# Kernel optimization log

Hardware: AMD Instinct MI355X
Metric: run time of the kernel (lower is better)

The kernel has to match this reference:

```python
import jax, jax.numpy as jnp
import numpy as np
from functools import partial

SEQ, B, IN, H, L = 2048, 48, 128, 256, 2


def _lstm_layer(x_seq, Wih, Whh, bih, bhh):
    # x_seq: [S, B, in_dim]; PyTorch gate order i, f, g, o along 4H axis.
    Bsz = x_seq.shape[1]
    h0 = jnp.zeros((Bsz, Whh.shape[1]), x_seq.dtype)
    c0 = jnp.zeros_like(h0)
    bias = bih + bhh

    def step(carry, x_t):
        h, c = carry
        gates = x_t @ Wih.T + h @ Whh.T + bias  # [B, 4H]
        i, f, g, o = jnp.split(gates, 4, axis=-1)
        i = jax.nn.sigmoid(i)
        f = jax.nn.sigmoid(f)
        g = jnp.tanh(g)
        o = jax.nn.sigmoid(o)
        c = f * c + i * g
        h = o * jnp.tanh(c)
        return (h, c), h

    (h_n, c_n), ys = jax.lax.scan(step, (h0, c0), x_seq)
    return ys, h_n


def setup_inputs() -> dict:
    key = jax.random.key(0)
    ks = jax.random.split(key, 11)
    s_in = 1.0 / np.sqrt(H)

    def u(k, shape):
        return jax.random.uniform(k, shape, jnp.float32, -s_in, s_in)

    return {
        "x": jax.random.normal(ks[0], (SEQ, B, IN), jnp.float32),
        "W_ih0": u(ks[1], (4 * H, IN)),
        "W_hh0": u(ks[2], (4 * H, H)),
        "b_ih0": u(ks[3], (4 * H,)),
        "b_hh0": u(ks[4], (4 * H,)),
        "W_ih1": u(ks[5], (4 * H, H)),
        "W_hh1": u(ks[6], (4 * H, H)),
        "b_ih1": u(ks[7], (4 * H,)),
        "b_hh1": u(ks[8], (4 * H,)),
        "fc_w": u(ks[9], (1, H)),
        "fc_b": u(ks[10], (1,)),
    }


def reference(x, W_ih0, W_hh0, b_ih0, b_hh0, W_ih1, W_hh1, b_ih1, b_hh1, fc_w, fc_b):
    y0, h0n = _lstm_layer(x, W_ih0, W_hh0, b_ih0, b_hh0)   # [S,B,H]
    y1, h1n = _lstm_layer(y0, W_ih1, W_hh1, b_ih1, b_hh1)  # [S,B,H]
    hn = jnp.stack([h0n, h1n], axis=0)                     # [L,B,H]
    # Original: output[:, -1, :] with batch_first=False => dim1 is BATCH,
    # so this selects the last batch element across all timesteps: [S, H].
    out = y1[:, -1, :] @ fc_w.T + fc_b                      # [S, 1]
    return (out, hn)
```

## Files before the change

### kernel.cpp

```cpp
#include <hip/hip_runtime.h>
#include <cstdint>
#include <cstddef>

#define SEQ   2048
#define BTOT  48
#define INDIM 128
#define HDIM  256
#define BG    16
#define NBG   3
#define USL   32
#define NMEM  8
#define NTHR  512

typedef short    bf16x8 __attribute__((ext_vector_type(8)));
typedef float    f32x4  __attribute__((ext_vector_type(4)));
typedef unsigned u32x4  __attribute__((ext_vector_type(4)));

__device__ __forceinline__ unsigned short f2bf(float f){
  union {float f; unsigned u;} v; v.f = f;
  unsigned r = v.u + 0x7fffu + ((v.u >> 16) & 1u);
  return (unsigned short)(r >> 16);
}
__device__ __forceinline__ float sigm(float xv){ return 1.0f/(1.0f + __expf(-xv)); }
__device__ __forceinline__ float tanh_(float xv){ return 1.0f - 2.0f/(__expf(2.0f*xv) + 1.0f); }

__device__ __forceinline__ void ld2x4_coh(const unsigned* p, u32x4& a, u32x4& b){
  asm volatile(
    "global_load_dwordx4 %0, %2, off sc0 sc1\n\t"
    "global_load_dwordx4 %1, %3, off sc0 sc1\n\t"
    "s_waitcnt vmcnt(0)"
    : "=v"(a), "=v"(b) : "v"(p), "v"(p+4) : "memory");
}
__device__ __forceinline__ void ld4x4_coh(const unsigned* p, const unsigned* q,
                                          u32x4& a, u32x4& b, u32x4& c, u32x4& d){
  asm volatile(
    "global_load_dwordx4 %0, %4, off sc0 sc1\n\t"
    "global_load_dwordx4 %1, %5, off sc0 sc1\n\t"
    "global_load_dwordx4 %2, %6, off sc0 sc1\n\t"
    "global_load_dwordx4 %3, %7, off sc0 sc1\n\t"
    "s_waitcnt vmcnt(0)"
    : "=v"(a), "=v"(b), "=v"(c), "=v"(d)
    : "v"(p), "v"(p+4), "v"(q), "v"(q+4) : "memory");
}
__device__ __forceinline__ void st_coh(unsigned* p, unsigned w){
  asm volatile("global_store_dword %0, %1, off sc0 sc1" :: "v"(p), "v"(w) : "memory");
}
__device__ __forceinline__ unsigned ld_coh(const unsigned* p){
  unsigned v;
  asm volatile("global_load_dword %0, %1, off sc0 sc1\n\ts_waitcnt vmcnt(0)"
               : "=v"(v) : "v"(p) : "memory");
  return v;
}
__device__ __forceinline__ int tags4(u32x4 a, unsigned want){
  return ((a[0]>>16)==want) & ((a[1]>>16)==want) & ((a[2]>>16)==want) & ((a[3]>>16)==want);
}
__device__ __forceinline__ u32x4 pack8(u32x4 a, u32x4 b){
  u32x4 r;
  r[0] = __builtin_amdgcn_perm(a[1], a[0], 0x05040100);
  r[1] = __builtin_amdgcn_perm(a[3], a[2], 0x05040100);
  r[2] = __builtin_amdgcn_perm(b[1], b[0], 0x05040100);
  r[3] = __builtin_amdgcn_perm(b[3], b[2], 0x05040100);
  return r;
}

template<int LAYER>
__device__ __forceinline__ void run_layer(
    const float* __restrict__ x,
    const float* __restrict__ Wih, const float* __restrict__ Whh,
    const float* __restrict__ bih, const float* __restrict__ bhh,
    unsigned* __restrict__ h0buf, unsigned* __restrict__ h1buf,
    unsigned* __restrict__ flags,
    float* __restrict__ y1buf, float* __restrict__ hn_out,
    int bg, int m, int D,
    char* __restrict__ smem_h, char* __restrict__ smem_x, float (*gacc)[132])
{
  const int Dm1  = D - 1;
  const int tid  = threadIdx.x;
  const int wave = tid >> 6;
  const int lane = tid & 63;
  const int l15  = lane & 15;
  const int krow = lane >> 4;
  const int u_base = m * USL;

  constexpr int KIH  = LAYER ? 256 : 128;
  constexpr int NKI  = KIH / 32;
  constexpr int NKT  = NKI + 8;
  constexpr int ROWB = LAYER ? 1024 : 512;

  const int jl    = wave*16 + l15;
  const int gg    = jl >> 5;
  const int ul    = jl & 31;
  const int jglob = gg*HDIM + u_base + ul;
  bf16x8 wfrag[NKT];
  #pragma unroll
  for (int kt = 0; kt < NKT; ++kt){
    const float* src = (kt < NKI)
        ? (Wih + (size_t)jglob*KIH + kt*32 + krow*8)
        : (Whh + (size_t)jglob*HDIM + (kt-NKI)*32 + krow*8);
    bf16x8 h8;
    #pragma unroll
    for (int i = 0; i < 8; ++i) h8[i] = (short)f2bf(src[i]);
    wfrag[kt] = h8;
  }

  const int ab = tid >> 5;
  const int au = tid & 31;
  const float bias0 = bih[0*HDIM + u_base + au] + bhh[0*HDIM + u_base + au];
  const float bias1 = bih[1*HDIM + u_base + au] + bhh[1*HDIM + u_base + au];
  const float bias2 = bih[2*HDIM + u_base + au] + bhh[2*HDIM + u_base + au];
  const float bias3 = bih[3*HDIM + u_base + au] + bhh[3*HDIM + u_base + au];
  float cst = 0.0f;

  const int sb  = tid >> 5;
  const int i32 = tid & 31;
  unsigned* prog = flags + bg*NMEM;
  const int swr = (sb & 7) << 4;
  const int swl = (l15 & 7) << 4;

  for (int s = 0; s < SEQ; ++s){
    const int wslot = s & Dm1;
    f32x4 acc = {0.f, 0.f, 0.f, 0.f};

    if (LAYER == 0){
      {
        const float4 xv = *(const float4*)(x + ((size_t)s*BTOT + bg*BG + sb)*INDIM + i32*4);
        uint2 wv;
        wv.x = (unsigned)f2bf(xv.x) | ((unsigned)f2bf(xv.y) << 16);
        wv.y = (unsigned)f2bf(xv.z) | ((unsigned)f2bf(xv.w) << 16);
        *(uint2*)(smem_x + sb*256 + ((i32*8) ^ swr)) = wv;
      }
      __syncthreads();
      #pragma unroll
      for (int kt = 0; kt < NKI; ++kt){
        bf16x8 af = *(const bf16x8*)(smem_x + l15*256 + ((kt*64 + krow*16) ^ swl));
        acc = __builtin_amdgcn_mfma_f32_16x16x32_bf16(af, wfrag[kt], acc, 0, 0, 0);
      }
      if (s > 0){
        const unsigned* ph = h0buf + (((size_t)((s-1) & Dm1)*NBG + bg)*BG + sb)*HDIM + i32*8;
        u32x4 a, b;
        do { ld2x4_coh(ph, a, b); } while (!(tags4(a, (unsigned)s) & tags4(b, (unsigned)s)));
        *(u32x4*)(smem_h + sb*ROWB + ((i32*16) ^ swr)) = pack8(a, b);
      }
      if (((s & 15) == 0) && (s + 16 > D)){
        const unsigned want = (unsigned)(s + 16 - D);
        const unsigned* p = prog + (tid & 7);
        while (ld_coh(p) < want) __builtin_amdgcn_s_sleep(2);
      }
      __syncthreads();
      if (s > 0){
        #pragma unroll
        for (int kt = 0; kt < 8; ++kt){
          bf16x8 af = *(const bf16x8*)(smem_h + l15*ROWB + ((kt*64 + krow*16) ^ swl));
          acc = __builtin_amdgcn_mfma_f32_16x16x32_bf16(af, wfrag[NKI+kt], acc, 0, 0, 0);
        }
      }
    } else {
      const unsigned* py = h0buf + (((size_t)wslot*NBG + bg)*BG + sb)*HDIM + i32*8;
      u32x4 a, b;
      if (s == 0){
        do { ld2x4_coh(py, a, b); } while (!(tags4(a, 1u) & tags4(b, 1u)));
      } else {
        const unsigned* ph = h1buf + (((size_t)((s-1) & Dm1)*NBG + bg)*BG + sb)*HDIM + i32*8;
        u32x4 c, d;
        do { ld4x4_coh(py, ph, a, b, c, d); }
        while (!(tags4(a, (unsigned)(s+1)) & tags4(b, (unsigned)(s+1))
               & tags4(c, (unsigned)s)     & tags4(d, (unsigned)s)));
        *(u32x4*)(smem_h + sb*ROWB + ((512 + i32*16) ^ swr)) = pack8(c, d);
      }
      *(u32x4*)(smem_h + sb*ROWB + ((i32*16) ^ swr)) = pack8(a, b);
      __syncthreads();
      #pragma unroll
      for (int kt = 0; kt < NKI; ++kt){
        bf16x8 af = *(const bf16x8*)(smem_h + l15*ROWB + ((kt*64 + krow*16) ^ swl));
        acc = __builtin_amdgcn_mfma_f32_16x16x32_bf16(af, wfrag[kt], acc, 0, 0, 0);
      }
      if (s > 0){
        #pragma unroll
        for (int kt = NKI; kt < NKT; ++kt){
          bf16x8 af = *(const bf16x8*)(smem_h + l15*ROWB + ((kt*64 + krow*16) ^ swl));
          acc = __builtin_amdgcn_mfma_f32_16x16x32_bf16(af, wfrag[kt], acc, 0, 0, 0);
        }
      }
    }

    #pragma unroll
    for (int r = 0; r < 4; ++r) gacc[krow*4 + r][wave*16 + l15] = acc[r];
    __syncthreads();

    {
      const float pi = gacc[ab][0*32 + au] + bias0;
      const float pf = gacc[ab][1*32 + au] + bias1;
      const float pg = gacc[ab][2*32 + au] + bias2;
      const float po = gacc[ab][3*32 + au] + bias3;
      const float iv = sigm(pi), fv = sigm(pf), gv = tanh_(pg), ov = sigm(po);
      cst = fv*cst + iv*gv;
      const float hv = ov * tanh_(cst);
      const unsigned word = (unsigned)f2bf(hv) | ((unsigned)(s+1) << 16);
      unsigned* dst = (LAYER ? h1buf : h0buf)
                    + (((size_t)wslot*NBG + bg)*BG + ab)*HDIM + u_base + au;
      st_coh(dst, word);
      if (LAYER == 1 && bg == 2 && ab == 15)
        y1buf[(size_t)s*HDIM + u_base + au] = hv;
      if (s == SEQ-1)
        hn_out[(size_t)LAYER*BTOT*HDIM + (size_t)(bg*BG + ab)*HDIM + u_base + au] = hv;
    }
    if (LAYER == 1 && tid == 0)
      st_coh(prog + m, (unsigned)(s+1));
  }
}

__global__ __launch_bounds__(NTHR, 1)
void lstm_main(const float* __restrict__ x,
               const float* __restrict__ Wih0, const float* __restrict__ Whh0,
               const float* __restrict__ bih0, const float* __restrict__ bhh0,
               const float* __restrict__ Wih1, const float* __restrict__ Whh1,
               const float* __restrict__ bih1, const float* __restrict__ bhh1,
               unsigned* h0buf, unsigned* h1buf, unsigned* flags,
               float* y1buf, float* hn_out, int D)
{
  __shared__ char  smem_h[16*1024];
  __shared__ char  smem_x[16*256];
  __shared__ float gacc[16][132];

  const int m  = blockIdx.x & 7;
  const int cl = blockIdx.x >> 3;
  const int bg = cl % 3;
  if (cl < 3)
    run_layer<0>(x, Wih0, Whh0, bih0, bhh0, h0buf, h1buf, flags,
                 y1buf, hn_out, bg, m, D, smem_h, smem_x, gacc);
  else
    run_layer<1>(x, Wih1, Whh1, bih1, bhh1, h0buf, h1buf, flags,
                 y1buf, hn_out, bg, m, D, smem_h, smem_x, gacc);
}

__global__ void lstm_out(const float* __restrict__ y1buf, const float* __restrict__ fcw,
                         const float* __restrict__ fcb, float* __restrict__ out)
{
  const int row  = blockIdx.x * 4 + (threadIdx.x >> 6);
  const int lane = threadIdx.x & 63;
  const float4 yv = *(const float4*)(y1buf + (size_t)row*HDIM + lane*4);
  const float4 wv = *(const float4*)(fcw + lane*4);
  float v = yv.x*wv.x + yv.y*wv.y + yv.z*wv.z + yv.w*wv.w;
  #pragma unroll
  for (int off = 32; off; off >>= 1) v += __shfl_down(v, off, 64);
  if (lane == 0) out[row] = v + fcb[0];
}

extern "C" void kernel_launch(void* const* d_in, const int* in_sizes, int n_in,
                              void* d_out, int out_size, void* d_ws, size_t ws_size,
                              hipStream_t stream)
{
  const float* x    = (const float*)d_in[0];
  const float* Wih0 = (const float*)d_in[1];
  const float* Whh0 = (const float*)d_in[2];
  const float* bih0 = (const float*)d_in[3];
  const float* bhh0 = (const float*)d_in[4];
  const float* Wih1 = (const float*)d_in[5];
  const float* Whh1 = (const float*)d_in[6];
  const float* bih1 = (const float*)d_in[7];
  const float* bhh1 = (const float*)d_in[8];
  const float* fcw  = (const float*)d_in[9];
  const float* fcb  = (const float*)d_in[10];
  float* out = (float*)d_out;

  int D = 64;
  while (D > 8){
    size_t need = 2*((size_t)D*NBG*BG*HDIM*4) + 4096 + (size_t)SEQ*HDIM*sizeof(float);
    if (need <= ws_size) break;
    D >>= 1;
  }
  char* p = (char*)d_ws;
  unsigned* h0buf = (unsigned*)p; p += (size_t)D*NBG*BG*HDIM*4;
  unsigned* h1buf = (unsigned*)p; p += (size_t)D*NBG*BG*HDIM*4;
  unsigned* flags = (unsigned*)p; p += 4096;
  float*    y1buf = (float*)p;

  hipMemsetAsync(d_ws, 0, 2*(size_t)D*NBG*BG*HDIM*4 + 4096, stream);

  hipLaunchKernelGGL(lstm_main, dim3(48), dim3(NTHR), 0, stream,
                     x, Wih0, Whh0, bih0, bhh0, Wih1, Whh1, bih1, bhh1,
                     h0buf, h1buf, flags, y1buf, out + SEQ, D);
  hipLaunchKernelGGL(lstm_out, dim3(SEQ/4), dim3(256), 0, stream,
                     y1buf, fcw, fcb, out);
}
```

Baseline: 5.614 ms.

## Co-locate each batch group on one XCD and poll L2-scoped buffers with fallback

The grid is enlarged and blocks are remapped so that all 16 workgroups of a batch group share blockIdx&7, which places them on the same XCD. Hidden-state exchange now writes twice: an L2-scoped copy that is polled with sc0 loads, and a system-coherent copy. Each workgroup falls back permanently to the coherent copy if polling fails for a bounded number of tries. This aims to cut the per-timestep cross-XCD synchronization latency. The change also prefetches the next x timestep, splits the MFMA chains across two accumulators, and drops the memset of the h buffers in favour of the tag scheme. The XCD placement it relies on is not guaranteed, it doubles the store traffic, and it needs more workspace.

```diff
diff --git a/kernel.cpp b/kernel.cpp
--- a/kernel.cpp
+++ b/kernel.cpp
@@ -11,6 +11,7 @@
 #define USL   32
 #define NMEM  8
 #define NTHR  512
+#define FAST_TRIES 1024
 
 typedef short    bf16x8 __attribute__((ext_vector_type(8)));
 typedef float    f32x4  __attribute__((ext_vector_type(4)));
@@ -24,28 +25,45 @@
 __device__ __forceinline__ float sigm(float xv){ return 1.0f/(1.0f + __expf(-xv)); }
 __device__ __forceinline__ float tanh_(float xv){ return 1.0f - 2.0f/(__expf(2.0f*xv) + 1.0f); }
 
-__device__ __forceinline__ void ld2x4_coh(const unsigned* p, u32x4& a, u32x4& b){
-  asm volatile(
-    "global_load_dwordx4 %0, %2, off sc0 sc1\n\t"
-    "global_load_dwordx4 %1, %3, off sc0 sc1\n\t"
-    "s_waitcnt vmcnt(0)"
-    : "=v"(a), "=v"(b) : "v"(p), "v"(p+4) : "memory");
-}
-__device__ __forceinline__ void ld4x4_coh(const unsigned* p, const unsigned* q,
-                                          u32x4& a, u32x4& b, u32x4& c, u32x4& d){
-  asm volatile(
-    "global_load_dwordx4 %0, %4, off sc0 sc1\n\t"
-    "global_load_dwordx4 %1, %5, off sc0 sc1\n\t"
-    "global_load_dwordx4 %2, %6, off sc0 sc1\n\t"
-    "global_load_dwordx4 %3, %7, off sc0 sc1\n\t"
-    "s_waitcnt vmcnt(0)"
-    : "=v"(a), "=v"(b), "=v"(c), "=v"(d)
-    : "v"(p), "v"(p+4), "v"(q), "v"(q+4) : "memory");
-}
-__device__ __forceinline__ void st_coh(unsigned* p, unsigned w){
+__device__ __forceinline__ void ld2x4_l2(const unsigned* p, u32x4& a, u32x4& b){
+  asm volatile("global_load_dwordx4 %0, %2, off sc0\n\t"
+               "global_load_dwordx4 %1, %3, off sc0\n\t"
+               "s_waitcnt vmcnt(0)"
+               : "=v"(a), "=v"(b) : "v"(p), "v"(p+4) : "memory");
+}
+__device__ __forceinline__ void ld2x4_ma(const unsigned* p, u32x4& a, u32x4& b){
+  asm volatile("global_load_dwordx4 %0, %2, off sc0 sc1\n\t"
+               "global_load_dwordx4 %1, %3, off sc0 sc1\n\t"
+               "s_waitcnt vmcnt(0)"
+               : "=v"(a), "=v"(b) : "v"(p), "v"(p+4) : "memory");
+}
+__device__ __forceinline__ void ld4x4_l2(const unsigned* p, const unsigned* q,
+                                         u32x4& a, u32x4& b, u32x4& c, u32x4& d){
+  asm volatile("global_load_dwordx4 %0, %4, off sc0\n\t"
+               "global_load_dwordx4 %1, %5, off sc0\n\t"
+               "global_load_dwordx4 %2, %6, off sc0\n\t"
+               "global_load_dwordx4 %3, %7, off sc0\n\t"
+               "s_waitcnt vmcnt(0)"
+               : "=v"(a), "=v"(b), "=v"(c), "=v"(d)
+               : "v"(p), "v"(p+4), "v"(q), "v"(q+4) : "memory");
+}
+__device__ __forceinline__ void ld4x4_ma(const unsigned* p, const unsigned* q,
+                                         u32x4& a, u32x4& b, u32x4& c, u32x4& d){
+  asm volatile("global_load_dwordx4 %0, %4, off sc0 sc1\n\t"
+               "global_load_dwordx4 %1, %5, off sc0 sc1\n\t"
+               "global_load_dwordx4 %2, %6, off sc0 sc1\n\t"
+               "global_load_dwordx4 %3, %7, off sc0 sc1\n\t"
+               "s_waitcnt vmcnt(0)"
+               : "=v"(a), "=v"(b), "=v"(c), "=v"(d)
+               : "v"(p), "v"(p+4), "v"(q), "v"(q+4) : "memory");
+}
+__device__ __forceinline__ void st_l2(unsigned* p, unsigned w){
+  asm volatile("global_store_dword %0, %1, off" :: "v"(p), "v"(w) : "memory");
+}
+__device__ __forceinline__ void st_ma(unsigned* p, unsigned w){
   asm volatile("global_store_dword %0, %1, off sc0 sc1" :: "v"(p), "v"(w) : "memory");
 }
-__device__ __forceinline__ unsigned ld_coh(const unsigned* p){
+__device__ __forceinline__ unsigned ld_ma1(const unsigned* p){
   unsigned v;
   asm volatile("global_load_dword %0, %1, off sc0 sc1\n\ts_waitcnt vmcnt(0)"
                : "=v"(v) : "v"(p) : "memory");
@@ -68,7 +86,8 @@
     const float* __restrict__ x,
     const float* __restrict__ Wih, const float* __restrict__ Whh,
     const float* __restrict__ bih, const float* __restrict__ bhh,
-    unsigned* __restrict__ h0buf, unsigned* __restrict__ h1buf,
+    unsigned* __restrict__ h0f, unsigned* __restrict__ h0s,
+    unsigned* __restrict__ h1f, unsigned* __restrict__ h1s,
     unsigned* __restrict__ flags,
     float* __restrict__ y1buf, float* __restrict__ hn_out,
     int bg, int m, int D,
@@ -117,13 +136,17 @@
   const int swr = (sb & 7) << 4;
   const int swl = (l15 & 7) << 4;
 
+  bool slowP = false;
+  float4 xv;
+  if (LAYER == 0)
+    xv = *(const float4*)(x + ((size_t)0*BTOT + bg*BG + sb)*INDIM + i32*4);
+
   for (int s = 0; s < SEQ; ++s){
     const int wslot = s & Dm1;
-    f32x4 acc = {0.f, 0.f, 0.f, 0.f};
+    f32x4 acc0 = {0.f,0.f,0.f,0.f}, acc1 = {0.f,0.f,0.f,0.f};
 
     if (LAYER == 0){
       {
-        const float4 xv = *(const float4*)(x + ((size_t)s*BTOT + bg*BG + sb)*INDIM + i32*4);
         uint2 wv;
         wv.x = (unsigned)f2bf(xv.x) | ((unsigned)f2bf(xv.y) << 16);
         wv.y = (unsigned)f2bf(xv.z) | ((unsigned)f2bf(xv.w) << 16);
@@ -133,38 +156,75 @@
       #pragma unroll
       for (int kt = 0; kt < NKI; ++kt){
         bf16x8 af = *(const bf16x8*)(smem_x + l15*256 + ((kt*64 + krow*16) ^ swl));
-        acc = __builtin_amdgcn_mfma_f32_16x16x32_bf16(af, wfrag[kt], acc, 0, 0, 0);
-      }
-      if (s > 0){
-        const unsigned* ph = h0buf + (((size_t)((s-1) & Dm1)*NBG + bg)*BG + sb)*HDIM + i32*8;
-        u32x4 a, b;
-        do { ld2x4_coh(ph, a, b); } while (!(tags4(a, (unsigned)s) & tags4(b, (unsigned)s)));
-        *(u32x4*)(smem_h + sb*ROWB + ((i32*16) ^ swr)) = pack8(a, b);
-      }
+        acc0 = __builtin_amdgcn_mfma_f32_16x16x32_bf16(af, wfrag[kt], acc0, 0, 0, 0);
+      }
+      if (s+1 < SEQ)
+        xv = *(const float4*)(x + ((size_t)(s+1)*BTOT + bg*BG + sb)*INDIM + i32*4);
       if (((s & 15) == 0) && (s + 16 > D)){
         const unsigned want = (unsigned)(s + 16 - D);
         const unsigned* p = prog + (tid & 7);
-        while (ld_coh(p) < want) __builtin_amdgcn_s_sleep(2);
+        while (ld_ma1(p) < want) __builtin_amdgcn_s_sleep(2);
+      }
+      if (s > 0){
+        const size_t off = (((size_t)((s-1) & Dm1)*NBG + bg)*BG + sb)*HDIM + i32*8;
+        const unsigned want = (unsigned)s;
+        u32x4 a, b;
+        if (!slowP){
+          int tries = FAST_TRIES;
+          for (;;){
+            ld2x4_l2(h0f + off, a, b);
+            if (tags4(a, want) & tags4(b, want)) break;
+            if (--tries == 0){ slowP = true; break; }
+          }
+        }
+        if (slowP){
+          do { ld2x4_ma(h0s + off, a, b); }
+          while (!(tags4(a, want) & tags4(b, want)));
+        }
+        *(u32x4*)(smem_h + sb*ROWB + ((i32*16) ^ swr)) = pack8(a, b);
       }
       __syncthreads();
       if (s > 0){
         #pragma unroll
         for (int kt = 0; kt < 8; ++kt){
           bf16x8 af = *(const bf16x8*)(smem_h + l15*ROWB + ((kt*64 + krow*16) ^ swl));
-          acc = __builtin_amdgcn_mfma_f32_16x16x32_bf16(af, wfrag[NKI+kt], acc, 0, 0, 0);
+          if (kt < 4) acc1 = __builtin_amdgcn_mfma_f32_16x16x32_bf16(af, wfrag[NKI+kt], acc1, 0, 0, 0);
+          else        acc0 = __builtin_amdgcn_mfma_f32_16x16x32_bf16(af, wfrag[NKI+kt], acc0, 0, 0, 0);
         }
       }
     } else {
-      const unsigned* py = h0buf + (((size_t)wslot*NBG + bg)*BG + sb)*HDIM + i32*8;
+      const size_t offy = (((size_t)wslot*NBG + bg)*BG + sb)*HDIM + i32*8;
+      const unsigned wy = (unsigned)(s+1);
       u32x4 a, b;
       if (s == 0){
-        do { ld2x4_coh(py, a, b); } while (!(tags4(a, 1u) & tags4(b, 1u)));
+        if (!slowP){
+          int tries = FAST_TRIES;
+          for (;;){
+            ld2x4_l2(h0f + offy, a, b);
+            if (tags4(a, wy) & tags4(b, wy)) break;
+            if (--tries == 0){ slowP = true; break; }
+          }
+        }
+        if (slowP){
+          do { ld2x4_ma(h0s + offy, a, b); }
+          while (!(tags4(a, wy) & tags4(b, wy)));
+        }
       } else {
-        const unsigned* ph = h1buf + (((size_t)((s-1) & Dm1)*NBG + bg)*BG + sb)*HDIM + i32*8;
+        const size_t offh = (((size_t)((s-1) & Dm1)*NBG + bg)*BG + sb)*HDIM + i32*8;
+        const unsigned wh = (unsigned)s;
         u32x4 c, d;
-        do { ld4x4_coh(py, ph, a, b, c, d); }
-        while (!(tags4(a, (unsigned)(s+1)) & tags4(b, (unsigned)(s+1))
-               & tags4(c, (unsigned)s)     & tags4(d, (unsigned)s)));
+        if (!slowP){
+          int tries = FAST_TRIES;
+          for (;;){
+            ld4x4_l2(h0f + offy, h1f + offh, a, b, c, d);
+            if (tags4(a, wy) & tags4(b, wy) & tags4(c, wh) & tags4(d, wh)) break;
+            if (--tries == 0){ slowP = true; break; }
+          }
+        }
+        if (slowP){
+          do { ld4x4_ma(h0s + offy, h1s + offh, a, b, c, d); }
+          while (!(tags4(a, wy) & tags4(b, wy) & tags4(c, wh) & tags4(d, wh)));
+        }
         *(u32x4*)(smem_h + sb*ROWB + ((512 + i32*16) ^ swr)) = pack8(c, d);
       }
       *(u32x4*)(smem_h + sb*ROWB + ((i32*16) ^ swr)) = pack8(a, b);
@@ -172,17 +232,20 @@
       #pragma unroll
       for (int kt = 0; kt < NKI; ++kt){
         bf16x8 af = *(const bf16x8*)(smem_h + l15*ROWB + ((kt*64 + krow*16) ^ swl));
-        acc = __builtin_amdgcn_mfma_f32_16x16x32_bf16(af, wfrag[kt], acc, 0, 0, 0);
+        if (kt & 1) acc1 = __builtin_amdgcn_mfma_f32_16x16x32_bf16(af, wfrag[kt], acc1, 0, 0, 0);
+        else        acc0 = __builtin_amdgcn_mfma_f32_16x16x32_bf16(af, wfrag[kt], acc0, 0, 0, 0);
       }
       if (s > 0){
         #pragma unroll
         for (int kt = NKI; kt < NKT; ++kt){
           bf16x8 af = *(const bf16x8*)(smem_h + l15*ROWB + ((kt*64 + krow*16) ^ swl));
-          acc = __builtin_amdgcn_mfma_f32_16x16x32_bf16(af, wfrag[kt], acc, 0, 0, 0);
+          if (kt & 1) acc1 = __builtin_amdgcn_mfma_f32_16x16x32_bf16(af, wfrag[kt], acc1, 0, 0, 0);
+          else        acc0 = __builtin_amdgcn_mfma_f32_16x16x32_bf16(af, wfrag[kt], acc0, 0, 0, 0);
         }
       }
     }
 
+    const f32x4 acc = acc0 + acc1;
     #pragma unroll
     for (int r = 0; r < 4; ++r) gacc[krow*4 + r][wave*16 + l15] = acc[r];
     __syncthreads();
@@ -196,16 +259,18 @@
       cst = fv*cst + iv*gv;
       const float hv = ov * tanh_(cst);
       const unsigned word = (unsigned)f2bf(hv) | ((unsigned)(s+1) << 16);
-      unsigned* dst = (LAYER ? h1buf : h0buf)
-                    + (((size_t)wslot*NBG + bg)*BG + ab)*HDIM + u_base + au;
-      st_coh(dst, word);
+      const size_t off = (((size_t)wslot*NBG + bg)*BG + ab)*HDIM + u_base + au;
+      unsigned* pf_ = (LAYER ? h1f : h0f) + off;
+      unsigned* ps_ = (LAYER ? h1s : h0s) + off;
+      st_l2(pf_, word);
+      st_ma(ps_, word);
       if (LAYER == 1 && bg == 2 && ab == 15)
         y1buf[(size_t)s*HDIM + u_base + au] = hv;
       if (s == SEQ-1)
         hn_out[(size_t)LAYER*BTOT*HDIM + (size_t)(bg*BG + ab)*HDIM + u_base + au] = hv;
     }
     if (LAYER == 1 && tid == 0)
-      st_coh(prog + m, (unsigned)(s+1));
+      st_ma(prog + m, (unsigned)(s+1));
   }
 }
 
@@ -215,21 +280,24 @@
                const float* __restrict__ bih0, const float* __restrict__ bhh0,
                const float* __restrict__ Wih1, const float* __restrict__ Whh1,
                const float* __restrict__ bih1, const float* __restrict__ bhh1,
-               unsigned* h0buf, unsigned* h1buf, unsigned* flags,
-               float* y1buf, float* hn_out, int D)
+               unsigned* h0f, unsigned* h0s, unsigned* h1f, unsigned* h1s,
+               unsigned* flags, float* y1buf, float* hn_out, int D)
 {
   __shared__ char  smem_h[16*1024];
   __shared__ char  smem_x[16*256];
   __shared__ float gacc[16][132];
 
-  const int m  = blockIdx.x & 7;
-  const int cl = blockIdx.x >> 3;
-  const int bg = cl % 3;
-  if (cl < 3)
-    run_layer<0>(x, Wih0, Whh0, bih0, bhh0, h0buf, h1buf, flags,
+  const int cls = blockIdx.x & 7;
+  if (cls >= NBG) return;
+  const int sub   = blockIdx.x >> 3;
+  const int layer = sub >> 3;
+  const int m     = sub & 7;
+  const int bg    = cls;
+  if (layer == 0)
+    run_layer<0>(x, Wih0, Whh0, bih0, bhh0, h0f, h0s, h1f, h1s, flags,
                  y1buf, hn_out, bg, m, D, smem_h, smem_x, gacc);
   else
-    run_layer<1>(x, Wih1, Whh1, bih1, bhh1, h0buf, h1buf, flags,
+    run_layer<1>(x, Wih1, Whh1, bih1, bhh1, h0f, h0s, h1f, h1s, flags,
                  y1buf, hn_out, bg, m, D, smem_h, smem_x, gacc);
 }
 
@@ -264,22 +332,24 @@
   float* out = (float*)d_out;
 
   int D = 64;
-  while (D > 8){
-    size_t need = 2*((size_t)D*NBG*BG*HDIM*4) + 4096 + (size_t)SEQ*HDIM*sizeof(float);
+  while (D > 16){
+    size_t need = 4*((size_t)D*NBG*BG*HDIM*4) + 4096 + (size_t)SEQ*HDIM*sizeof(float);
     if (need <= ws_size) break;
     D >>= 1;
   }
   char* p = (char*)d_ws;
-  unsigned* h0buf = (unsigned*)p; p += (size_t)D*NBG*BG*HDIM*4;
-  unsigned* h1buf = (unsigned*)p; p += (size_t)D*NBG*BG*HDIM*4;
+  unsigned* h0f   = (unsigned*)p; p += (size_t)D*NBG*BG*HDIM*4;
+  unsigned* h0s   = (unsigned*)p; p += (size_t)D*NBG*BG*HDIM*4;
+  unsigned* h1f   = (unsigned*)p; p += (size_t)D*NBG*BG*HDIM*4;
+  unsigned* h1s   = (unsigned*)p; p += (size_t)D*NBG*BG*HDIM*4;
   unsigned* flags = (unsigned*)p; p += 4096;
   float*    y1buf = (float*)p;
 
-  hipMemsetAsync(d_ws, 0, 2*(size_t)D*NBG*BG*HDIM*4 + 4096, stream);
-
-  hipLaunchKernelGGL(lstm_main, dim3(48), dim3(NTHR), 0, stream,
+  (void)hipMemsetAsync(flags, 0, 4096, stream);
+
+  hipLaunchKernelGGL(lstm_main, dim3(128), dim3(NTHR), 0, stream,
                      x, Wih0, Whh0, bih0, bhh0, Wih1, Whh1, bih1, bhh1,
-                     h0buf, h1buf, flags, y1buf, out + SEQ, D);
+                     h0f, h0s, h1f, h1s, flags, y1buf, out + SEQ, D);
   hipLaunchKernelGGL(lstm_out, dim3(SEQ/4), dim3(256), 0, stream,
                      y1buf, fcw, fcb, out);
 }
```

Result: slower. 9.938 ms (+77.0%).
